# Kernel optimization log

Hardware: AMD Instinct MI355X
Metric: run time of the kernel (lower is better)

The kernel has to match this reference:

```python
import jax, jax.numpy as jnp
import numpy as np

D_MODEL = 1024
D_STATE = 16
D_CONV = 4
EXPAND = 2
D_INNER = EXPAND * D_MODEL  # 2048
DT_RANK = 64
B, L = 1, 1024


def setup_inputs() -> dict:
    key = jax.random.key(0)
    ks = jax.random.split(key, 10)
    s = 0.02
    x = jax.random.normal(ks[0], (B, L, D_MODEL), dtype=jnp.float32)
    in_proj_w = jax.random.normal(ks[1], (2 * D_INNER, D_MODEL), dtype=jnp.float32) * s
    conv_w = jax.random.normal(ks[2], (D_INNER, 1, D_CONV), dtype=jnp.float32) * s
    conv_b = jax.random.normal(ks[3], (D_INNER,), dtype=jnp.float32) * s
    x_proj_w = jax.random.normal(ks[4], (DT_RANK + 2 * D_STATE, D_INNER), dtype=jnp.float32) * s
    dt_init_std = DT_RANK ** (-0.5)
    dt_proj_w = jax.random.uniform(ks[5], (D_INNER, DT_RANK), dtype=jnp.float32,
                                   minval=-dt_init_std, maxval=dt_init_std)
    dt = jnp.exp(jax.random.uniform(ks[6], (D_INNER,), dtype=jnp.float32)
                 * (np.log(0.1) - np.log(0.001)) + np.log(0.001))
    dt = jnp.clip(dt, 1e-4, None)
    dt_proj_b = dt + jnp.log(-jnp.expm1(-dt))  # inverse softplus
    A_log = jnp.log(jnp.broadcast_to(jnp.arange(1, D_STATE + 1, dtype=jnp.float32),
                                     (D_INNER, D_STATE)))
    D = jnp.ones((D_INNER,), dtype=jnp.float32)
    out_proj_w = jax.random.normal(ks[7], (D_MODEL, D_INNER), dtype=jnp.float32) * s
    return {"x": x, "in_proj_w": in_proj_w, "conv_w": conv_w, "conv_b": conv_b,
            "x_proj_w": x_proj_w, "dt_proj_w": dt_proj_w, "dt_proj_b": dt_proj_b,
            "A_log": A_log, "D": D, "out_proj_w": out_proj_w}


def _selective_scan(u, delta, A, Bm, Cm, Dv):
    # u, delta: [b,l,d]; A: [d,n]; Bm, Cm: [b,l,n]; Dv: [d]
    deltaA = jnp.exp(jnp.einsum('bld,dn->bldn', delta, A))           # [b,l,d,n]
    deltaB_u = jnp.einsum('bld,bld,bln->bldn', delta, u, Bm)          # [b,l,d,n]
    xs = (jnp.swapaxes(deltaA, 0, 1), jnp.swapaxes(deltaB_u, 0, 1),
          jnp.swapaxes(Cm, 0, 1))  # time-major

    def step(state, inp):
        dA_t, dBu_t, C_t = inp               # [b,d,n], [b,d,n], [b,n]
        state = dA_t * state + dBu_t
        y_t = jnp.einsum('bdn,bn->bd', state, C_t)
        return state, y_t

    state0 = jnp.zeros((u.shape[0], u.shape[2], A.shape[1]), dtype=u.dtype)
    _, ys = jax.lax.scan(step, state0, xs)    # ys: [l,b,d]
    y = jnp.swapaxes(ys, 0, 1)
    return y + u * Dv


def reference(x, in_proj_w, conv_w, conv_b, x_proj_w, dt_proj_w, dt_proj_b,
              A_log, D, out_proj_w):
    b, l, _ = x.shape
    xz = x @ in_proj_w.T                      # [b,l,2*d_inner]
    xi, z = jnp.split(xz, 2, axis=-1)
    # causal depthwise conv1d (pad left d_conv-1, truncate to L)
    xc = jnp.swapaxes(xi, 1, 2)               # [b,d_inner,l]
    xc = jax.lax.conv_general_dilated(
        xc, conv_w, window_strides=(1,), padding=[(D_CONV - 1, 0)],
        dimension_numbers=('NCH', 'OIH', 'NCH'), feature_group_count=D_INNER)
    xc = xc + conv_b[None, :, None]
    xi = jax.nn.silu(jnp.swapaxes(xc, 1, 2))  # [b,l,d_inner]
    # SSM
    A = -jnp.exp(A_log)
    x_dbl = xi @ x_proj_w.T                   # [b,l,dt_rank+2n]
    delta, Bm, Cm = jnp.split(x_dbl, [DT_RANK, DT_RANK + D_STATE], axis=-1)
    delta = jax.nn.softplus(delta @ dt_proj_w.T + dt_proj_b)
    y = _selective_scan(xi, delta, A, Bm, Cm, D)
    y = y * jax.nn.silu(z)
    return y @ out_proj_w.T
```

## Files before the change

### kernel.cpp

```cpp
#include <hip/hip_runtime.h>
#include <hip/hip_bf16.h>
#include <cstdint>
#include <cstddef>


typedef __attribute__((ext_vector_type(4))) float f32x4;
typedef __attribute__((ext_vector_type(8))) short short8;

#define GLOAD_LDS16(g, l)                                                      \
  __builtin_amdgcn_global_load_lds(                                            \
      (const __attribute__((address_space(1))) void*)(g),                      \
      (__attribute__((address_space(3))) void*)(l), 16, 0, 0)

__device__ __forceinline__ unsigned short f2bf(float f) {
  union { float f; unsigned u; } v; v.f = f;
  unsigned u = v.u;
  unsigned r = (u + 0x7FFFu + ((u >> 16) & 1u)) >> 16;
  return (unsigned short)r;
}

__global__ __launch_bounds__(256) void convert_all(
    const float* __restrict__ a0, unsigned short* __restrict__ o0, int n0,
    const float* __restrict__ a1, unsigned short* __restrict__ o1, int n1,
    const float* __restrict__ a2, unsigned short* __restrict__ o2, int n2,
    const float* __restrict__ a3, unsigned short* __restrict__ o3, int n3,
    const float* __restrict__ a4, unsigned short* __restrict__ o4, int n4) {
  const float* a; unsigned short* o; int n;
  switch (blockIdx.y) {
    case 0: a = a0; o = o0; n = n0; break;
    case 1: a = a1; o = o1; n = n1; break;
    case 2: a = a2; o = o2; n = n2; break;
    case 3: a = a3; o = o3; n = n3; break;
    default: a = a4; o = o4; n = n4; break;
  }
  int n4c = n >> 2;
  int stride = gridDim.x * blockDim.x;
  for (int i = blockIdx.x * blockDim.x + threadIdx.x; i < n4c; i += stride) {
    float4 v = ((const float4*)a)[i];
    uint2 p;
    p.x = (unsigned)f2bf(v.x) | ((unsigned)f2bf(v.y) << 16);
    p.y = (unsigned)f2bf(v.z) | ((unsigned)f2bf(v.w) << 16);
    ((uint2*)o)[i] = p;
  }
}

template <int SPLITK>
__global__ __launch_bounds__(256) void gemm64(
    const unsigned short* __restrict__ A, const unsigned short* __restrict__ B,
    float* __restrict__ C, int M, int N, int K) {
  __shared__ unsigned short lds[2][2][64 * 64];
  const int tid  = threadIdx.x;
  const int lane = tid & 63;
  const int w    = tid >> 6;
  const int mBase = blockIdx.y * 64;
  const int nBase = blockIdx.x * 64;
  const int kLen  = K / SPLITK;
  const int kBase = (SPLITK > 1) ? blockIdx.z * kLen : 0;
  const int wr = (w >> 1) * 32;
  const int wc = (w & 1) * 32;
  const int wchunk = tid & 192;

  f32x4 acc[2][2];
  #pragma unroll
  for (int m = 0; m < 2; ++m)
    #pragma unroll
    for (int n = 0; n < 2; ++n)
      acc[m][n] = (f32x4){0.f, 0.f, 0.f, 0.f};

  auto stage = [&](int b, int k0) {
    #pragma unroll
    for (int j = 0; j < 2; ++j) {
      int chunk = tid + j * 256;
      int row = chunk >> 3;
      int t = chunk & 7;
      int col = (t ^ (row & 7)) * 8;
      GLOAD_LDS16(&A[(size_t)(mBase + row) * K + k0 + col],
                  &lds[b][0][(size_t)(wchunk + j * 256) * 8]);
      GLOAD_LDS16(&B[(size_t)(nBase + row) * K + k0 + col],
                  &lds[b][1][(size_t)(wchunk + j * 256) * 8]);
    }
  };

  const int kIters = kLen / 64;
  stage(0, kBase);
  __syncthreads();
  int buf = 0;
  for (int it = 0; it < kIters; ++it) {
    if (it + 1 < kIters) stage(buf ^ 1, kBase + (it + 1) * 64);
    short8 af[2][2], bfr[2][2];
    #pragma unroll
    for (int m = 0; m < 2; ++m)
      #pragma unroll
      for (int kk = 0; kk < 2; ++kk) {
        int row = wr + m * 16 + (lane & 15);
        int s = kk * 4 + (lane >> 4);
        af[m][kk] = *(const short8*)&lds[buf][0][row * 64 + ((s ^ (row & 7)) * 8)];
      }
    #pragma unroll
    for (int n = 0; n < 2; ++n)
      #pragma unroll
      for (int kk = 0; kk < 2; ++kk) {
        int row = wc + n * 16 + (lane & 15);
        int s = kk * 4 + (lane >> 4);
        bfr[n][kk] = *(const short8*)&lds[buf][1][row * 64 + ((s ^ (row & 7)) * 8)];
      }
    #pragma unroll
    for (int kk = 0; kk < 2; ++kk)
      #pragma unroll
      for (int m = 0; m < 2; ++m)
        #pragma unroll
        for (int n = 0; n < 2; ++n)
          acc[m][n] = __builtin_amdgcn_mfma_f32_16x16x32_bf16(
              af[m][kk], bfr[n][kk], acc[m][n], 0, 0, 0);
    __syncthreads();
    buf ^= 1;
  }

  float* Co = C + (SPLITK > 1 ? (size_t)blockIdx.z * M * N : (size_t)0);
  #pragma unroll
  for (int m = 0; m < 2; ++m) {
    int row0 = mBase + wr + m * 16 + (lane >> 4) * 4;
    #pragma unroll
    for (int n = 0; n < 2; ++n) {
      int col = nBase + wc + n * 16 + (lane & 15);
      #pragma unroll
      for (int r = 0; r < 4; ++r)
        Co[(size_t)(row0 + r) * N + col] = acc[m][n][r];
    }
  }
}

__global__ __launch_bounds__(256) void reduce2(
    const float* __restrict__ P, float* __restrict__ out, int n4) {
  int i = blockIdx.x * 256 + threadIdx.x;
  if (i < n4) {
    f32x4 a = ((const f32x4*)P)[i];
    f32x4 b = ((const f32x4*)P)[i + n4];
    ((f32x4*)out)[i] = a + b;
  }
}

__global__ __launch_bounds__(256) void conv_silu(
    const float* __restrict__ xz, const float* __restrict__ cw,
    const float* __restrict__ cb, float* __restrict__ xi_f,
    unsigned short* __restrict__ xi_b) {
  int d = blockIdx.x * 256 + threadIdx.x;
  int l = blockIdx.y;
  float acc = cb[d];
  #pragma unroll
  for (int k = 0; k < 4; ++k) {
    int ll = l - 3 + k;
    if (ll >= 0) acc += xz[(size_t)ll * 4096 + d] * cw[d * 4 + k];
  }
  float s = acc / (1.f + __expf(-acc));
  xi_f[(size_t)l * 2048 + d] = s;
  xi_b[(size_t)l * 2048 + d] = f2bf(s);
}

__global__ __launch_bounds__(256) void xproj(
    const unsigned short* __restrict__ xi_b, const unsigned short* __restrict__ xw_b,
    unsigned short* __restrict__ xd_b, float* __restrict__ Bm, float* __restrict__ Cm) {
  __shared__ f32x4 red[4][64];
  int tid = threadIdx.x, lane = tid & 63, w = tid >> 6;
  int mt = blockIdx.x, nt = blockIdx.y;
  int arow = mt * 16 + (lane & 15);
  int brow = nt * 16 + (lane & 15);
  int kg = (lane >> 4) * 8;
  f32x4 acc = (f32x4){0.f, 0.f, 0.f, 0.f};
  for (int k0 = w * 512; k0 < (w + 1) * 512; k0 += 32) {
    short8 a = *(const short8*)&xi_b[(size_t)arow * 2048 + k0 + kg];
    short8 b = *(const short8*)&xw_b[(size_t)brow * 2048 + k0 + kg];
    acc = __builtin_amdgcn_mfma_f32_16x16x32_bf16(a, b, acc, 0, 0, 0);
  }
  red[w][lane] = acc;
  __syncthreads();
  if (w == 0) {
    acc = red[0][lane];
    acc += red[1][lane];
    acc += red[2][lane];
    acc += red[3][lane];
    int ocol = nt * 16 + (lane & 15);
    #pragma unroll
    for (int r = 0; r < 4; ++r) {
      int row = mt * 16 + (lane >> 4) * 4 + r;
      float v = acc[r];
      if (ocol < 64)      xd_b[row * 64 + ocol] = f2bf(v);
      else if (ocol < 80) Bm[row * 16 + (ocol - 64)] = v;
      else                Cm[row * 16 + (ocol - 80)] = v;
    }
  }
}

__global__ __launch_bounds__(64) void dtproj(
    const unsigned short* __restrict__ xd_b, const unsigned short* __restrict__ dtw_b,
    const float* __restrict__ dtb, float* __restrict__ delta) {
  int lane = threadIdx.x;
  int mt = blockIdx.x, nt = blockIdx.y;
  int arow = mt * 16 + (lane & 15);
  int brow = nt * 16 + (lane & 15);
  int kg = (lane >> 4) * 8;
  f32x4 acc = (f32x4){0.f, 0.f, 0.f, 0.f};
  #pragma unroll
  for (int k0 = 0; k0 < 64; k0 += 32) {
    short8 a = *(const short8*)&xd_b[arow * 64 + k0 + kg];
    short8 b = *(const short8*)&dtw_b[brow * 64 + k0 + kg];
    acc = __builtin_amdgcn_mfma_f32_16x16x32_bf16(a, b, acc, 0, 0, 0);
  }
  int ocol = nt * 16 + (lane & 15);
  float bias = dtb[ocol];
  #pragma unroll
  for (int r = 0; r < 4; ++r) {
    int row = mt * 16 + (lane >> 4) * 4 + r;
    float v = acc[r] + bias;
    float sp = (v > 20.f) ? v : log1pf(__expf(v));
    delta[(size_t)row * 2048 + ocol] = sp;
  }
}

__global__ __launch_bounds__(64) void scan_p1(
    const float* __restrict__ delta, const float* __restrict__ xi_f,
    const float* __restrict__ Bm, const float* __restrict__ A_log,
    float* __restrict__ P, float* __restrict__ S) {
  int d = blockIdx.x * 64 + threadIdx.x;
  int c = blockIdx.y;
  float a[16], p[16], s[16];
  #pragma unroll
  for (int n = 0; n < 16; ++n) {
    a[n] = -__expf(A_log[d * 16 + n]);
    p[n] = 1.f; s[n] = 0.f;
  }
  for (int t = 0; t < 32; ++t) {
    int l = c * 32 + t;
    float dl = delta[(size_t)l * 2048 + d];
    float u  = xi_f[(size_t)l * 2048 + d];
    float du = dl * u;
    float bv[16];
    *(float4*)(bv + 0)  = *(const float4*)&Bm[l * 16 + 0];
    *(float4*)(bv + 4)  = *(const float4*)&Bm[l * 16 + 4];
    *(float4*)(bv + 8)  = *(const float4*)&Bm[l * 16 + 8];
    *(float4*)(bv + 12) = *(const float4*)&Bm[l * 16 + 12];
    #pragma unroll
    for (int n = 0; n < 16; ++n) {
      float dA = __expf(dl * a[n]);
      s[n] = fmaf(dA, s[n], du * bv[n]);
      p[n] *= dA;
    }
  }
  #pragma unroll
  for (int n = 0; n < 16; ++n) {
    P[(size_t)(c * 16 + n) * 2048 + d] = p[n];
    S[(size_t)(c * 16 + n) * 2048 + d] = s[n];
  }
}

__global__ __launch_bounds__(256) void scan_p2(
    const float* __restrict__ P, const float* __restrict__ S,
    float* __restrict__ SIn) {
  int idx = blockIdx.x * 256 + threadIdx.x;
  float sin_ = 0.f;
  for (int c = 0; c < 32; ++c) {
    SIn[c * 32768 + idx] = sin_;
    sin_ = fmaf(P[c * 32768 + idx], sin_, S[c * 32768 + idx]);
  }
}

__global__ __launch_bounds__(64) void scan_p3(
    const float* __restrict__ delta, const float* __restrict__ xi_f,
    const float* __restrict__ Bm, const float* __restrict__ Cm,
    const float* __restrict__ A_log, const float* __restrict__ Dv,
    const float* __restrict__ SIn, const float* __restrict__ xz,
    unsigned short* __restrict__ y_b) {
  int d = blockIdx.x * 64 + threadIdx.x;
  int c = blockIdx.y;
  float a[16], s[16];
  #pragma unroll
  for (int n = 0; n < 16; ++n) {
    a[n] = -__expf(A_log[d * 16 + n]);
    s[n] = SIn[c * 32768 + n * 2048 + d];
  }
  float Dd = Dv[d];
  for (int t = 0; t < 32; ++t) {
    int l = c * 32 + t;
    float dl = delta[(size_t)l * 2048 + d];
    float u  = xi_f[(size_t)l * 2048 + d];
    float du = dl * u;
    float bv[16], cv[16];
    *(float4*)(bv + 0)  = *(const float4*)&Bm[l * 16 + 0];
    *(float4*)(bv + 4)  = *(const float4*)&Bm[l * 16 + 4];
    *(float4*)(bv + 8)  = *(const float4*)&Bm[l * 16 + 8];
    *(float4*)(bv + 12) = *(const float4*)&Bm[l * 16 + 12];
    *(float4*)(cv + 0)  = *(const float4*)&Cm[l * 16 + 0];
    *(float4*)(cv + 4)  = *(const float4*)&Cm[l * 16 + 4];
    *(float4*)(cv + 8)  = *(const float4*)&Cm[l * 16 + 8];
    *(float4*)(cv + 12) = *(const float4*)&Cm[l * 16 + 12];
    float y = 0.f;
    #pragma unroll
    for (int n = 0; n < 16; ++n) {
      float dA = __expf(dl * a[n]);
      s[n] = fmaf(dA, s[n], du * bv[n]);
      y = fmaf(s[n], cv[n], y);
    }
    y = fmaf(u, Dd, y);
    float zz = xz[(size_t)l * 4096 + 2048 + d];
    float sig = 1.f / (1.f + __expf(-zz));
    y *= zz * sig;
    y_b[(size_t)l * 2048 + d] = f2bf(y);
  }
}

extern "C" void kernel_launch(void* const* d_in, const int* in_sizes, int n_in,
                              void* d_out, int out_size, void* d_ws, size_t ws_size,
                              hipStream_t stream) {
  const float* x      = (const float*)d_in[0];
  const float* Win    = (const float*)d_in[1];
  const float* convw  = (const float*)d_in[2];
  const float* convb  = (const float*)d_in[3];
  const float* xprojw = (const float*)d_in[4];
  const float* dtw    = (const float*)d_in[5];
  const float* dtb    = (const float*)d_in[6];
  const float* Alog   = (const float*)d_in[7];
  const float* Dv     = (const float*)d_in[8];
  const float* Wout   = (const float*)d_in[9];
  float* out = (float*)d_out;

  char* ws = (char*)d_ws;
  size_t off = 0;
  auto alloc = [&](size_t bytes) -> void* {
    void* p = ws + off;
    off = (off + bytes + 255) & ~(size_t)255;
    return p;
  };
  unsigned short* x_bf    = (unsigned short*)alloc((size_t)1024 * 1024 * 2);
  unsigned short* Win_bf  = (unsigned short*)alloc((size_t)4096 * 1024 * 2);
  unsigned short* Wout_bf = (unsigned short*)alloc((size_t)1024 * 2048 * 2);
  unsigned short* xw_bf   = (unsigned short*)alloc((size_t)96 * 2048 * 2);
  unsigned short* dtw_bf  = (unsigned short*)alloc((size_t)2048 * 64 * 2);
  float* xz               = (float*)alloc((size_t)1024 * 4096 * 4);
  float* xi_f             = (float*)alloc((size_t)1024 * 2048 * 4);
  unsigned short* xi_bf   = (unsigned short*)alloc((size_t)1024 * 2048 * 2);
  unsigned short* xd_bf   = (unsigned short*)alloc((size_t)1024 * 64 * 2);
  float* Bm               = (float*)alloc((size_t)1024 * 16 * 4);
  float* Cm               = (float*)alloc((size_t)1024 * 16 * 4);
  float* delta            = (float*)alloc((size_t)1024 * 2048 * 4);
  float* P                = (float*)alloc((size_t)32 * 16 * 2048 * 4);
  float* S                = (float*)alloc((size_t)32 * 16 * 2048 * 4);
  float* SIn              = (float*)alloc((size_t)32 * 16 * 2048 * 4);
  unsigned short* y_bf    = (unsigned short*)alloc((size_t)1024 * 2048 * 2);

  convert_all<<<dim3(512, 5), 256, 0, stream>>>(
      x, x_bf, 1024 * 1024,
      Win, Win_bf, 4096 * 1024,
      Wout, Wout_bf, 1024 * 2048,
      xprojw, xw_bf, 96 * 2048,
      dtw, dtw_bf, 2048 * 64);
  gemm64<1><<<dim3(64, 16), 256, 0, stream>>>(x_bf, Win_bf, xz, 1024, 4096, 1024);
  conv_silu<<<dim3(8, 1024), 256, 0, stream>>>(xz, convw, convb, xi_f, xi_bf);
  xproj<<<dim3(64, 6), 256, 0, stream>>>(xi_bf, xw_bf, xd_bf, Bm, Cm);
  dtproj<<<dim3(64, 128), 64, 0, stream>>>(xd_bf, dtw_bf, dtb, delta);
  scan_p1<<<dim3(32, 32), 64, 0, stream>>>(delta, xi_f, Bm, Alog, P, S);
  scan_p2<<<dim3(128), 256, 0, stream>>>(P, S, SIn);
  scan_p3<<<dim3(32, 32), 64, 0, stream>>>(delta, xi_f, Bm, Cm, Alog, Dv, SIn, xz, y_bf);
  gemm64<2><<<dim3(16, 16, 2), 256, 0, stream>>>(y_bf, Wout_bf, P, 1024, 1024, 2048);
  reduce2<<<dim3(1024), 256, 0, stream>>>(P, out, 262144);
}
```

Measured before the change: 117.9 us.

## Store xz and xi in bf16, vectorize conv, remap GEMM blocks per XCD, batch scan loads

The in_proj GEMM now writes its output in bf16 instead of fp32. conv_silu now reads bf16, handles 8 channels by 4 timesteps per thread with vector loads, and stops writing the fp32 copy of xi. Both scans read u and z in bf16 and batch several timesteps of loads per iteration, and GEMM blocks are remapped so neighbouring tiles share an XCD for L2 locality. These changes cut memory traffic, at the cost of precision in the z gate and in u inside the scan.

```diff
diff --git a/kernel.cpp b/kernel.cpp
--- a/kernel.cpp
+++ b/kernel.cpp
@@ -17,6 +17,10 @@
   unsigned u = v.u;
   unsigned r = (u + 0x7FFFu + ((u >> 16) & 1u)) >> 16;
   return (unsigned short)r;
+}
+__device__ __forceinline__ float bf2f(unsigned short u) {
+  union { unsigned u; float f; } v; v.u = ((unsigned)u) << 16;
+  return v.f;
 }
 
 __global__ __launch_bounds__(256) void convert_all(
@@ -44,18 +48,28 @@
   }
 }
 
-template <int SPLITK>
+template <int SPLITK, int OBF>
 __global__ __launch_bounds__(256) void gemm64(
     const unsigned short* __restrict__ A, const unsigned short* __restrict__ B,
-    float* __restrict__ C, int M, int N, int K) {
+    void* __restrict__ Cv, int M, int N, int K) {
   __shared__ unsigned short lds[2][2][64 * 64];
   const int tid  = threadIdx.x;
   const int lane = tid & 63;
   const int w    = tid >> 6;
-  const int mBase = blockIdx.y * 64;
-  const int nBase = blockIdx.x * 64;
+
+  const int nx = gridDim.x, ny = gridDim.y;
+  int l = (blockIdx.z * ny + blockIdx.y) * nx + blockIdx.x;
+  int xcd = l & 7, idx = l >> 3;
+  int by = idx % ny;
+  int r_ = idx / ny;
+  int slab = nx >> 3;
+  int bx = xcd * slab + (r_ % slab);
+  int bz = r_ / slab;
+
+  const int mBase = by * 64;
+  const int nBase = bx * 64;
   const int kLen  = K / SPLITK;
-  const int kBase = (SPLITK > 1) ? blockIdx.z * kLen : 0;
+  const int kBase = (SPLITK > 1) ? bz * kLen : 0;
   const int wr = (w >> 1) * 32;
   const int wc = (w & 1) * 32;
   const int wchunk = tid & 192;
@@ -116,16 +130,31 @@
     buf ^= 1;
   }
 
-  float* Co = C + (SPLITK > 1 ? (size_t)blockIdx.z * M * N : (size_t)0);
-  #pragma unroll
-  for (int m = 0; m < 2; ++m) {
-    int row0 = mBase + wr + m * 16 + (lane >> 4) * 4;
-    #pragma unroll
-    for (int n = 0; n < 2; ++n) {
-      int col = nBase + wc + n * 16 + (lane & 15);
-      #pragma unroll
-      for (int r = 0; r < 4; ++r)
-        Co[(size_t)(row0 + r) * N + col] = acc[m][n][r];
+  if (OBF) {
+    unsigned short* Cb = (unsigned short*)Cv;
+    #pragma unroll
+    for (int m = 0; m < 2; ++m) {
+      int row0 = mBase + wr + m * 16 + (lane >> 4) * 4;
+      #pragma unroll
+      for (int n = 0; n < 2; ++n) {
+        int col = nBase + wc + n * 16 + (lane & 15);
+        #pragma unroll
+        for (int r = 0; r < 4; ++r)
+          Cb[(size_t)(row0 + r) * N + col] = f2bf(acc[m][n][r]);
+      }
+    }
+  } else {
+    float* Co = (float*)Cv + (SPLITK > 1 ? (size_t)bz * M * N : (size_t)0);
+    #pragma unroll
+    for (int m = 0; m < 2; ++m) {
+      int row0 = mBase + wr + m * 16 + (lane >> 4) * 4;
+      #pragma unroll
+      for (int n = 0; n < 2; ++n) {
+        int col = nBase + wc + n * 16 + (lane & 15);
+        #pragma unroll
+        for (int r = 0; r < 4; ++r)
+          Co[(size_t)(row0 + r) * N + col] = acc[m][n][r];
+      }
     }
   }
 }
@@ -141,20 +170,42 @@
 }
 
 __global__ __launch_bounds__(256) void conv_silu(
-    const float* __restrict__ xz, const float* __restrict__ cw,
-    const float* __restrict__ cb, float* __restrict__ xi_f,
-    unsigned short* __restrict__ xi_b) {
-  int d = blockIdx.x * 256 + threadIdx.x;
-  int l = blockIdx.y;
-  float acc = cb[d];
-  #pragma unroll
-  for (int k = 0; k < 4; ++k) {
-    int ll = l - 3 + k;
-    if (ll >= 0) acc += xz[(size_t)ll * 4096 + d] * cw[d * 4 + k];
-  }
-  float s = acc / (1.f + __expf(-acc));
-  xi_f[(size_t)l * 2048 + d] = s;
-  xi_b[(size_t)l * 2048 + d] = f2bf(s);
+    const unsigned short* __restrict__ xz_bf, const float* __restrict__ cw,
+    const float* __restrict__ cb, unsigned short* __restrict__ xi_b) {
+  int d0 = threadIdx.x * 8;
+  int l0 = blockIdx.x * 4;
+  float wgt[8][4], bias[8];
+  #pragma unroll
+  for (int j = 0; j < 8; ++j) {
+    float4 t = *(const float4*)&cw[(d0 + j) * 4];
+    wgt[j][0] = t.x; wgt[j][1] = t.y; wgt[j][2] = t.z; wgt[j][3] = t.w;
+  }
+  *(float4*)(bias + 0) = *(const float4*)&cb[d0];
+  *(float4*)(bias + 4) = *(const float4*)&cb[d0 + 4];
+
+  short8 rows[7];
+  #pragma unroll
+  for (int r = 0; r < 7; ++r) {
+    int ll = l0 - 3 + r;
+    if (ll >= 0)
+      rows[r] = *(const short8*)&xz_bf[(size_t)ll * 4096 + d0];
+    else
+      rows[r] = (short8){0, 0, 0, 0, 0, 0, 0, 0};
+  }
+  #pragma unroll
+  for (int q = 0; q < 4; ++q) {
+    short8 outv;
+    #pragma unroll
+    for (int j = 0; j < 8; ++j) {
+      float acc = bias[j];
+      #pragma unroll
+      for (int k = 0; k < 4; ++k)
+        acc = fmaf(bf2f((unsigned short)rows[q + k][j]), wgt[j][k], acc);
+      float s = acc / (1.f + __expf(-acc));
+      outv[j] = (short)f2bf(s);
+    }
+    *(short8*)&xi_b[(size_t)(l0 + q) * 2048 + d0] = outv;
+  }
 }
 
 __global__ __launch_bounds__(256) void xproj(
@@ -218,7 +269,7 @@
 }
 
 __global__ __launch_bounds__(64) void scan_p1(
-    const float* __restrict__ delta, const float* __restrict__ xi_f,
+    const float* __restrict__ delta, const unsigned short* __restrict__ xi_b,
     const float* __restrict__ Bm, const float* __restrict__ A_log,
     float* __restrict__ P, float* __restrict__ S) {
   int d = blockIdx.x * 64 + threadIdx.x;
@@ -229,21 +280,27 @@
     a[n] = -__expf(A_log[d * 16 + n]);
     p[n] = 1.f; s[n] = 0.f;
   }
-  for (int t = 0; t < 32; ++t) {
-    int l = c * 32 + t;
-    float dl = delta[(size_t)l * 2048 + d];
-    float u  = xi_f[(size_t)l * 2048 + d];
-    float du = dl * u;
-    float bv[16];
-    *(float4*)(bv + 0)  = *(const float4*)&Bm[l * 16 + 0];
-    *(float4*)(bv + 4)  = *(const float4*)&Bm[l * 16 + 4];
-    *(float4*)(bv + 8)  = *(const float4*)&Bm[l * 16 + 8];
-    *(float4*)(bv + 12) = *(const float4*)&Bm[l * 16 + 12];
-    #pragma unroll
-    for (int n = 0; n < 16; ++n) {
-      float dA = __expf(dl * a[n]);
-      s[n] = fmaf(dA, s[n], du * bv[n]);
-      p[n] *= dA;
+  for (int tb = 0; tb < 8; ++tb) {
+    int l0 = c * 32 + tb * 4;
+    float dl[4], uu[4], bv[4][16];
+    #pragma unroll
+    for (int q = 0; q < 4; ++q) {
+      dl[q] = delta[(size_t)(l0 + q) * 2048 + d];
+      uu[q] = bf2f(xi_b[(size_t)(l0 + q) * 2048 + d]);
+      *(float4*)(bv[q] + 0)  = *(const float4*)&Bm[(l0 + q) * 16 + 0];
+      *(float4*)(bv[q] + 4)  = *(const float4*)&Bm[(l0 + q) * 16 + 4];
+      *(float4*)(bv[q] + 8)  = *(const float4*)&Bm[(l0 + q) * 16 + 8];
+      *(float4*)(bv[q] + 12) = *(const float4*)&Bm[(l0 + q) * 16 + 12];
+    }
+    #pragma unroll
+    for (int q = 0; q < 4; ++q) {
+      float du = dl[q] * uu[q];
+      #pragma unroll
+      for (int n = 0; n < 16; ++n) {
+        float dA = __expf(dl[q] * a[n]);
+        s[n] = fmaf(dA, s[n], du * bv[q][n]);
+        p[n] *= dA;
+      }
     }
   }
   #pragma unroll
@@ -258,6 +315,7 @@
     float* __restrict__ SIn) {
   int idx = blockIdx.x * 256 + threadIdx.x;
   float sin_ = 0.f;
+  #pragma unroll 8
   for (int c = 0; c < 32; ++c) {
     SIn[c * 32768 + idx] = sin_;
     sin_ = fmaf(P[c * 32768 + idx], sin_, S[c * 32768 + idx]);
@@ -265,10 +323,10 @@
 }
 
 __global__ __launch_bounds__(64) void scan_p3(
-    const float* __restrict__ delta, const float* __restrict__ xi_f,
+    const float* __restrict__ delta, const unsigned short* __restrict__ xi_b,
     const float* __restrict__ Bm, const float* __restrict__ Cm,
     const float* __restrict__ A_log, const float* __restrict__ Dv,
-    const float* __restrict__ SIn, const float* __restrict__ xz,
+    const float* __restrict__ SIn, const unsigned short* __restrict__ xz_bf,
     unsigned short* __restrict__ y_b) {
   int d = blockIdx.x * 64 + threadIdx.x;
   int c = blockIdx.y;
@@ -279,32 +337,39 @@
     s[n] = SIn[c * 32768 + n * 2048 + d];
   }
   float Dd = Dv[d];
-  for (int t = 0; t < 32; ++t) {
-    int l = c * 32 + t;
-    float dl = delta[(size_t)l * 2048 + d];
-    float u  = xi_f[(size_t)l * 2048 + d];
-    float du = dl * u;
-    float bv[16], cv[16];
-    *(float4*)(bv + 0)  = *(const float4*)&Bm[l * 16 + 0];
-    *(float4*)(bv + 4)  = *(const float4*)&Bm[l * 16 + 4];
-    *(float4*)(bv + 8)  = *(const float4*)&Bm[l * 16 + 8];
-    *(float4*)(bv + 12) = *(const float4*)&Bm[l * 16 + 12];
-    *(float4*)(cv + 0)  = *(const float4*)&Cm[l * 16 + 0];
-    *(float4*)(cv + 4)  = *(const float4*)&Cm[l * 16 + 4];
-    *(float4*)(cv + 8)  = *(const float4*)&Cm[l * 16 + 8];
-    *(float4*)(cv + 12) = *(const float4*)&Cm[l * 16 + 12];
-    float y = 0.f;
-    #pragma unroll
-    for (int n = 0; n < 16; ++n) {
-      float dA = __expf(dl * a[n]);
-      s[n] = fmaf(dA, s[n], du * bv[n]);
-      y = fmaf(s[n], cv[n], y);
-    }
-    y = fmaf(u, Dd, y);
-    float zz = xz[(size_t)l * 4096 + 2048 + d];
-    float sig = 1.f / (1.f + __expf(-zz));
-    y *= zz * sig;
-    y_b[(size_t)l * 2048 + d] = f2bf(y);
+  for (int tb = 0; tb < 16; ++tb) {
+    int l0 = c * 32 + tb * 2;
+    float dl[2], uu[2], zz[2], bv[2][16], cv[2][16];
+    #pragma unroll
+    for (int q = 0; q < 2; ++q) {
+      int l = l0 + q;
+      dl[q] = delta[(size_t)l * 2048 + d];
+      uu[q] = bf2f(xi_b[(size_t)l * 2048 + d]);
+      zz[q] = bf2f(xz_bf[(size_t)l * 4096 + 2048 + d]);
+      *(float4*)(bv[q] + 0)  = *(const float4*)&Bm[l * 16 + 0];
+      *(float4*)(bv[q] + 4)  = *(const float4*)&Bm[l * 16 + 4];
+      *(float4*)(bv[q] + 8)  = *(const float4*)&Bm[l * 16 + 8];
+      *(float4*)(bv[q] + 12) = *(const float4*)&Bm[l * 16 + 12];
+      *(float4*)(cv[q] + 0)  = *(const float4*)&Cm[l * 16 + 0];
+      *(float4*)(cv[q] + 4)  = *(const float4*)&Cm[l * 16 + 4];
+      *(float4*)(cv[q] + 8)  = *(const float4*)&Cm[l * 16 + 8];
+      *(float4*)(cv[q] + 12) = *(const float4*)&Cm[l * 16 + 12];
+    }
+    #pragma unroll
+    for (int q = 0; q < 2; ++q) {
+      float du = dl[q] * uu[q];
+      float y = 0.f;
+      #pragma unroll
+      for (int n = 0; n < 16; ++n) {
+        float dA = __expf(dl[q] * a[n]);
+        s[n] = fmaf(dA, s[n], du * bv[q][n]);
+        y = fmaf(s[n], cv[q][n], y);
+      }
+      y = fmaf(uu[q], Dd, y);
+      float sig = 1.f / (1.f + __expf(-zz[q]));
+      y *= zz[q] * sig;
+      y_b[(size_t)(l0 + q) * 2048 + d] = f2bf(y);
+    }
   }
 }
 
@@ -335,8 +400,7 @@
   unsigned short* Wout_bf = (unsigned short*)alloc((size_t)1024 * 2048 * 2);
   unsigned short* xw_bf   = (unsigned short*)alloc((size_t)96 * 2048 * 2);
   unsigned short* dtw_bf  = (unsigned short*)alloc((size_t)2048 * 64 * 2);
-  float* xz               = (float*)alloc((size_t)1024 * 4096 * 4);
-  float* xi_f             = (float*)alloc((size_t)1024 * 2048 * 4);
+  unsigned short* xz_bf   = (unsigned short*)alloc((size_t)1024 * 4096 * 2);
   unsigned short* xi_bf   = (unsigned short*)alloc((size_t)1024 * 2048 * 2);
   unsigned short* xd_bf   = (unsigned short*)alloc((size_t)1024 * 64 * 2);
   float* Bm               = (float*)alloc((size_t)1024 * 16 * 4);
@@ -353,13 +417,13 @@
       Wout, Wout_bf, 1024 * 2048,
       xprojw, xw_bf, 96 * 2048,
       dtw, dtw_bf, 2048 * 64);
-  gemm64<1><<<dim3(64, 16), 256, 0, stream>>>(x_bf, Win_bf, xz, 1024, 4096, 1024);
-  conv_silu<<<dim3(8, 1024), 256, 0, stream>>>(xz, convw, convb, xi_f, xi_bf);
+  gemm64<1, 1><<<dim3(64, 16), 256, 0, stream>>>(x_bf, Win_bf, xz_bf, 1024, 4096, 1024);
+  conv_silu<<<dim3(256), 256, 0, stream>>>(xz_bf, convw, convb, xi_bf);
   xproj<<<dim3(64, 6), 256, 0, stream>>>(xi_bf, xw_bf, xd_bf, Bm, Cm);
   dtproj<<<dim3(64, 128), 64, 0, stream>>>(xd_bf, dtw_bf, dtb, delta);
-  scan_p1<<<dim3(32, 32), 64, 0, stream>>>(delta, xi_f, Bm, Alog, P, S);
+  scan_p1<<<dim3(32, 32), 64, 0, stream>>>(delta, xi_bf, Bm, Alog, P, S);
   scan_p2<<<dim3(128), 256, 0, stream>>>(P, S, SIn);
-  scan_p3<<<dim3(32, 32), 64, 0, stream>>>(delta, xi_f, Bm, Cm, Alog, Dv, SIn, xz, y_bf);
-  gemm64<2><<<dim3(16, 16, 2), 256, 0, stream>>>(y_bf, Wout_bf, P, 1024, 1024, 2048);
+  scan_p3<<<dim3(32, 32), 64, 0, stream>>>(delta, xi_bf, Bm, Cm, Alog, Dv, SIn, xz_bf, y_bf);
+  gemm64<2, 0><<<dim3(16, 16, 2), 256, 0, stream>>>(y_bf, Wout_bf, P, 1024, 1024, 2048);
   reduce2<<<dim3(1024), 256, 0, stream>>>(P, out, 262144);
 }
```

Result: faster. 109.6 us (-7.1%).
